# Performance work log

Measured on AMD Instinct MI355X. Metric: run time of the kernel, lower is better.

Reference implementation:

```python
import jax, jax.numpy as jnp
from jax import lax
import numpy as np

NUM_CLASSES = 80
STRIDE = 8
TOPK = 100
SIGAMA = 8.0


def setup_inputs() -> dict:
    key = jax.random.key(0)
    # raw head output: [B, 4+num_classes, H, W]
    x = jax.random.normal(key, (16, 4 + NUM_CLASSES, 160, 160), dtype=jnp.float32)
    return {"input": x}


def _decode(input):
    bs, attrs, H, W = input.shape
    C = attrs - 4
    pred = jnp.transpose(input, (0, 2, 3, 1))  # [B,H,W,4+C]
    x = jax.nn.sigmoid(pred[..., 0])
    y = jax.nn.sigmoid(pred[..., 1])
    w = pred[..., 2]
    h = pred[..., 3]
    pred_cls = jax.nn.sigmoid(pred[..., 4:])  # [B,H,W,C]

    grid_x = jnp.arange(W, dtype=input.dtype)[None, None, :]
    grid_y = jnp.arange(H, dtype=input.dtype)[None, :, None]
    pred_boxes = jnp.stack(
        [x + grid_x, y + grid_y, jnp.exp(w) * SIGAMA, jnp.exp(h) * SIGAMA], axis=-1
    )  # [B,H,W,4]

    # Faithful to F.max_pool2d applied to a [B,H,W,C] tensor: torch pools the
    # LAST TWO dims, i.e. a 5x5 window over (W, C), padding 2, stride 1.
    neg_inf = jnp.array(-jnp.inf, dtype=pred_cls.dtype)
    hmax = lax.reduce_window(
        pred_cls, neg_inf, lax.max,
        window_dimensions=(1, 1, 5, 5),
        window_strides=(1, 1, 1, 1),
        padding=((0, 0), (0, 0), (2, 2), (2, 2)),
    )
    keep = (hmax == pred_cls).astype(pred_cls.dtype)
    pred_cls = pred_cls * keep

    # --- dual top-k (CenterNet-style) ---
    scores = jnp.transpose(pred_cls, (0, 3, 1, 2)).reshape(bs, C, H * W)
    topk_scores, topk_inds = lax.top_k(scores, TOPK)          # [B,C,K] per-class
    topk_score, topk_ind = lax.top_k(topk_scores.reshape(bs, C * TOPK), TOPK)  # [B,K]
    topk_clses = (topk_ind // TOPK).astype(jnp.int32)         # class of each pick
    topk_inds = jnp.take_along_axis(topk_inds.reshape(bs, C * TOPK), topk_ind, axis=1)  # [B,K] spatial idx

    boxes = jnp.take_along_axis(
        pred_boxes.reshape(bs, H * W, 4), topk_inds[:, :, None], axis=1
    )  # [B,K,4]
    cls = jnp.take_along_axis(
        pred_cls.reshape(bs, H * W, C), topk_inds[:, :, None], axis=1
    )  # [B,K,C]
    conf = jnp.ones((bs, TOPK, 1), dtype=input.dtype)
    scale = jnp.array([STRIDE, STRIDE, STRIDE, STRIDE], dtype=input.dtype)
    return jnp.concatenate([boxes * scale, conf, cls], axis=-1)  # [B,K,5+C]


def reference(input):
    return _decode(input)
```

## Files before the change

kernel.cpp:

```cpp
#include <hip/hip_runtime.h>
#include <hip/hip_bf16.h>
#include <cstdint>

#define BATCH 16
#define ATTRS 84
#define NC    80
#define HH    160
#define WW    160
#define HWSZ  (HH * WW)
#define KTOP  100
#define CAP   8192
#define XGATE 2.9444389791664403f
#define LDW   48
#define LCAP  64
#define CSTR  16

__device__ __forceinline__ float sigf(float x) {
    return 1.0f / (1.0f + __expf(-x));
}

__global__ __launch_bounds__(320, 8) void k_nms(const float* __restrict__ in,
                                                unsigned long long* __restrict__ gather,
                                                unsigned int* __restrict__ counts) {
    const int wg  = blockIdx.x;
    const int b   = wg / (HH * 4);
    const int rem = wg % (HH * 4);
    const int h   = rem >> 2;
    const int q   = rem & 3;
    const int t   = (int)threadIdx.x;

    __shared__ float sg[NC][LDW];
    __shared__ unsigned long long lbuf[LCAP];
    __shared__ unsigned int lcount;
    __shared__ unsigned int gbase;

    if (t == 0) lcount = 0;

    const int w0 = q * 40;
    const float* slab = in + ((size_t)b * ATTRS + 4) * HWSZ + (size_t)h * WW + (w0 - 4);

#pragma unroll
    for (int it = 0; it < 3; ++it) {
        const int f4 = it * 320 + t;
        const int c  = f4 / 12;
        const int j4 = f4 % 12;
        const bool oob = (q == 0 && j4 == 0) || (q == 3 && j4 == 11);
        float4 v;
        if (oob) {
            v.x = -INFINITY; v.y = -INFINITY; v.z = -INFINITY; v.w = -INFINITY;
        } else {
            v = *reinterpret_cast<const float4*>(slab + (size_t)c * HWSZ + j4 * 4);
        }
        *reinterpret_cast<float4*>(&sg[c][j4 * 4]) = v;
    }
    __syncthreads();

    const int c    = t % NC;
    const int wq2  = t / NC;
    const int cj0  = 4 + wq2 * 10;

    float s_[14];
#pragma unroll
    for (int k = 0; k < 7; ++k) {
        const float2 v2 = *reinterpret_cast<const float2*>(&sg[c][cj0 - 2 + 2 * k]);
        s_[2 * k + 0] = v2.x;
        s_[2 * k + 1] = v2.y;
    }

    const int r0 = max(c - 2, 0), r1 = max(c - 1, 0);
    const int r3 = min(c + 1, NC - 1), r4 = min(c + 2, NC - 1);

#pragma unroll
    for (int i = 0; i < 10; ++i) {
        const float x = s_[i + 2];
        if (x >= XGATE) {
            const int j = cj0 + i;
            float vm = -INFINITY;
#pragma unroll
            for (int dj = -2; dj <= 2; ++dj) {
                const int jj = j + dj;
                vm = fmaxf(vm, sg[r0][jj]);
                vm = fmaxf(vm, sg[r1][jj]);
                vm = fmaxf(vm, sg[c ][jj]);
                vm = fmaxf(vm, sg[r3][jj]);
                vm = fmaxf(vm, sg[r4][jj]);
            }
            if (x == vm) {
                const float ssc = sigf(x);
                const int w = w0 + wq2 * 10 + i;
                const unsigned idx = (unsigned)(c * HWSZ + h * WW + w);
                unsigned long long key =
                    ((unsigned long long)__float_as_uint(ssc) << 21) |
                    (unsigned long long)(0x1FFFFFu - idx);
                unsigned p = atomicAdd(&lcount, 1u);
                if (p < LCAP) {
                    lbuf[p] = key;
                } else {
                    unsigned g = atomicAdd(&counts[b * CSTR], 1u);
                    if (g < CAP) gather[(size_t)b * CAP + g] = key;
                }
            }
        }
    }
    __syncthreads();

    const unsigned n = min(lcount, (unsigned)LCAP);
    if (t == 0 && n > 0) gbase = atomicAdd(&counts[b * CSTR], n);
    __syncthreads();
    for (unsigned i = t; i < n; i += 320) {
        unsigned g = gbase + i;
        if (g < CAP) gather[(size_t)b * CAP + g] = lbuf[i];
    }
}

__global__ __launch_bounds__(256) void k_select(const unsigned long long* __restrict__ gather,
                                                const unsigned int* __restrict__ counts,
                                                unsigned int* __restrict__ picks) {
    const int b = blockIdx.x;
    const int t = (int)threadIdx.x;

    __shared__ unsigned int hist[2048];
    __shared__ unsigned int chunksum[256];
    __shared__ unsigned long long compact[512];
    __shared__ unsigned int ncompact;
    __shared__ int b2_sh;

    const int M = min(counts[b * CSTR], (unsigned)CAP);
    const unsigned long long* keys = gather + (size_t)b * CAP;

    for (int i = t; i < 2048; i += 256) hist[i] = 0;
    if (t == 0) ncompact = 0;
    __syncthreads();

    for (int i = t; i < M; i += 256) {
        unsigned sb = (unsigned)(keys[i] >> 21);
        int bk = (int)((sb - 0x3F700000u) >> 9);
        bk = min(max(bk, 0), 2047);
        atomicAdd(&hist[bk], 1u);
    }
    __syncthreads();

    unsigned sum = 0;
#pragma unroll
    for (int j = 0; j < 8; ++j) sum += hist[t * 8 + j];
    chunksum[t] = sum;
    __syncthreads();
    for (int off = 1; off < 256; off <<= 1) {
        unsigned v = (t + off < 256) ? chunksum[t + off] : 0u;
        __syncthreads();
        chunksum[t] += v;
        __syncthreads();
    }

    const int target = (M < KTOP) ? M : KTOP;
    if (target > 0 &&
        (int)chunksum[t] >= target && (t == 255 || (int)chunksum[t + 1] < target)) {
        unsigned cum = (t == 255) ? 0u : chunksum[t + 1];
        int bsel = t * 8;
        for (int j = 7; j >= 0; --j) {
            cum += hist[t * 8 + j];
            if ((int)cum >= target) { bsel = t * 8 + j; break; }
        }
        b2_sh = bsel;
    }
    __syncthreads();
    const int b2 = b2_sh;

    for (int i = t; i < M; i += 256) {
        unsigned long long k = keys[i];
        unsigned sb = (unsigned)(k >> 21);
        int bk = min(max((int)((sb - 0x3F700000u) >> 9), 0), 2047);
        if (bk >= b2) {
            unsigned p = atomicAdd(&ncompact, 1u);
            if (p < 512) compact[p] = k;
        }
    }
    __syncthreads();

    const int N = (int)min(ncompact, 512u);
    for (int i = t; i < N; i += 256) {
        unsigned long long ki = compact[i];
        int rank = 0;
        for (int j = 0; j < N; ++j) rank += (compact[j] > ki) ? 1 : 0;
        if (rank < KTOP) {
            unsigned idx = 0x1FFFFFu - (unsigned)(ki & 0x1FFFFFu);
            picks[b * KTOP + rank] = idx % HWSZ;
        }
    }
}

__global__ __launch_bounds__(128) void k_emit(const float* __restrict__ in,
                                              const unsigned int* __restrict__ picks,
                                              float* __restrict__ out) {
    const int pk = blockIdx.x;
    const int b  = pk / KTOP;
    const int t  = (int)threadIdx.x;
    const unsigned hw = picks[pk];
    const int h = (int)(hw / WW), w = (int)(hw % WW);

    __shared__ float tile[NC][5];

    const float* base = in + (size_t)b * ATTRS * HWSZ;

    if (t < NC) {
        const int c = t;
        int a0 = (max(w - 2, 0)) & ~3;
        a0 = min(a0, WW - 8);
        const float* rp = base + (size_t)(4 + c) * HWSZ + (size_t)h * WW;
        const float4 f0 = *reinterpret_cast<const float4*>(rp + a0);
        const float4 f1 = *reinterpret_cast<const float4*>(rp + a0 + 4);
        float sp[8] = { f0.x, f0.y, f0.z, f0.w, f1.x, f1.y, f1.z, f1.w };
#pragma unroll
        for (int j = 0; j < 5; ++j) {
            const int wc = w + j - 2;
            float vv = -INFINITY;
            if (wc >= 0 && wc < WW) vv = sigf(sp[wc - a0]);
            tile[c][j] = vv;
        }
    }
    __syncthreads();

    float* orow = out + (size_t)pk * (5 + NC);

    if (t < 4) {
        float v = base[(size_t)t * HWSZ + hw];
        float r;
        if (t == 0)      r = (sigf(v) + (float)w) * 8.0f;
        else if (t == 1) r = (sigf(v) + (float)h) * 8.0f;
        else             r = expf(v) * 64.0f;
        orow[t] = r;
    }
    if (t == 4) orow[4] = 1.0f;

    if (t < NC) {
        const int c = t;
        const int cl = max(0, c - 2), ch = min(NC - 1, c + 2);
        float m = -INFINITY;
        for (int cc = cl; cc <= ch; ++cc) {
#pragma unroll
            for (int j = 0; j < 5; ++j) m = fmaxf(m, tile[cc][j]);
        }
        float sc = tile[c][2];
        orow[5 + c] = (sc == m) ? sc : 0.0f;
    }
}

extern "C" void kernel_launch(void* const* d_in, const int* in_sizes, int n_in,
                              void* d_out, int out_size, void* d_ws, size_t ws_size,
                              hipStream_t stream) {
    const float* in = (const float*)d_in[0];
    float* out = (float*)d_out;

    unsigned int* counts = (unsigned int*)d_ws;
    unsigned int* picks  = (unsigned int*)((char*)d_ws + 1024);
    unsigned long long* gather = (unsigned long long*)((char*)d_ws + 8192);

    hipMemsetAsync(d_ws, 0, 1024, stream);

    k_nms<<<BATCH * HH * 4, 320, 0, stream>>>(in, gather, counts);
    k_select<<<BATCH, 256, 0, stream>>>(gather, counts, picks);
    k_emit<<<BATCH * KTOP, 128, 0, stream>>>(in, picks, out);
}
```

Before: 230.5 us.

## Stream class planes with flat float4 reads and check rare candidates from global

Replaces the LDS-staged slab NMS, where each workgroup covered one row quarter across all 80 classes, with a flat streaming pass: each workgroup reads a contiguous 64KB chunk of class scores as coalesced float4 loads. Only values above the sigmoid gate (about 0.15% of elements) trigger a 5x5 window check, which reads neighbours straight from global memory through the caches. This removes the strided per-class slab loads, the shared-memory staging and a barrier, and uses far fewer, larger workgroups. The cost is scattered, divergent global reads for candidates and a larger local key buffer.

```diff
diff --git a/kernel.cpp b/kernel.cpp
--- a/kernel.cpp
+++ b/kernel.cpp
@@ -11,93 +11,69 @@
 #define KTOP  100
 #define CAP   8192
 #define XGATE 2.9444389791664403f
-#define LDW   48
-#define LCAP  64
+#define LCAP  192
 #define CSTR  16
+#define CHUNKS 125
 
 __device__ __forceinline__ float sigf(float x) {
     return 1.0f / (1.0f + __expf(-x));
 }
 
-__global__ __launch_bounds__(320, 8) void k_nms(const float* __restrict__ in,
-                                                unsigned long long* __restrict__ gather,
-                                                unsigned int* __restrict__ counts) {
-    const int wg  = blockIdx.x;
-    const int b   = wg / (HH * 4);
-    const int rem = wg % (HH * 4);
-    const int h   = rem >> 2;
-    const int q   = rem & 3;
-    const int t   = (int)threadIdx.x;
-
-    __shared__ float sg[NC][LDW];
+__global__ __launch_bounds__(256) void k_nms(const float* __restrict__ in,
+                                             unsigned long long* __restrict__ gather,
+                                             unsigned int* __restrict__ counts) {
+    const int wg    = blockIdx.x;
+    const int b     = wg / CHUNKS;
+    const int chunk = wg % CHUNKS;
+    const int t     = (int)threadIdx.x;
+
     __shared__ unsigned long long lbuf[LCAP];
     __shared__ unsigned int lcount;
     __shared__ unsigned int gbase;
 
     if (t == 0) lcount = 0;
-
-    const int w0 = q * 40;
-    const float* slab = in + ((size_t)b * ATTRS + 4) * HWSZ + (size_t)h * WW + (w0 - 4);
-
-#pragma unroll
-    for (int it = 0; it < 3; ++it) {
-        const int f4 = it * 320 + t;
-        const int c  = f4 / 12;
-        const int j4 = f4 % 12;
-        const bool oob = (q == 0 && j4 == 0) || (q == 3 && j4 == 11);
-        float4 v;
-        if (oob) {
-            v.x = -INFINITY; v.y = -INFINITY; v.z = -INFINITY; v.w = -INFINITY;
-        } else {
-            v = *reinterpret_cast<const float4*>(slab + (size_t)c * HWSZ + j4 * 4);
-        }
-        *reinterpret_cast<float4*>(&sg[c][j4 * 4]) = v;
-    }
-    __syncthreads();
-
-    const int c    = t % NC;
-    const int wq2  = t / NC;
-    const int cj0  = 4 + wq2 * 10;
-
-    float s_[14];
-#pragma unroll
-    for (int k = 0; k < 7; ++k) {
-        const float2 v2 = *reinterpret_cast<const float2*>(&sg[c][cj0 - 2 + 2 * k]);
-        s_[2 * k + 0] = v2.x;
-        s_[2 * k + 1] = v2.y;
-    }
-
-    const int r0 = max(c - 2, 0), r1 = max(c - 1, 0);
-    const int r3 = min(c + 1, NC - 1), r4 = min(c + 2, NC - 1);
-
-#pragma unroll
-    for (int i = 0; i < 10; ++i) {
-        const float x = s_[i + 2];
-        if (x >= XGATE) {
-            const int j = cj0 + i;
-            float vm = -INFINITY;
-#pragma unroll
-            for (int dj = -2; dj <= 2; ++dj) {
-                const int jj = j + dj;
-                vm = fmaxf(vm, sg[r0][jj]);
-                vm = fmaxf(vm, sg[r1][jj]);
-                vm = fmaxf(vm, sg[c ][jj]);
-                vm = fmaxf(vm, sg[r3][jj]);
-                vm = fmaxf(vm, sg[r4][jj]);
-            }
-            if (x == vm) {
-                const float ssc = sigf(x);
-                const int w = w0 + wq2 * 10 + i;
-                const unsigned idx = (unsigned)(c * HWSZ + h * WW + w);
-                unsigned long long key =
-                    ((unsigned long long)__float_as_uint(ssc) << 21) |
-                    (unsigned long long)(0x1FFFFFu - idx);
-                unsigned p = atomicAdd(&lcount, 1u);
-                if (p < LCAP) {
-                    lbuf[p] = key;
-                } else {
-                    unsigned g = atomicAdd(&counts[b * CSTR], 1u);
-                    if (g < CAP) gather[(size_t)b * CAP + g] = key;
+    __syncthreads();
+
+    const float* slab = in + ((size_t)b * ATTRS + 4) * HWSZ;
+    const int base_f4 = chunk * 4096;
+
+#pragma unroll
+    for (int it = 0; it < 16; ++it) {
+        const int f4 = base_f4 + it * 256 + t;
+        const float4 v = *reinterpret_cast<const float4*>(slab + (size_t)f4 * 4);
+        const float vmax = fmaxf(fmaxf(v.x, v.y), fmaxf(v.z, v.w));
+        if (vmax >= XGATE) {
+#pragma unroll
+            for (int jj = 0; jj < 4; ++jj) {
+                const float x = (&v.x)[jj];
+                if (x >= XGATE) {
+                    const int f = f4 * 4 + jj;
+                    const int c = f / HWSZ;
+                    const int r = f % HWSZ;
+                    const int h = r / WW;
+                    const int w = r % WW;
+                    const int c0 = max(c - 2, 0), c1 = min(c + 2, NC - 1);
+                    const int wl = max(w - 2, 0), wh = min(w + 2, WW - 1);
+                    float vm = -INFINITY;
+                    for (int cc = c0; cc <= c1; ++cc) {
+                        const float* rowp = slab + (size_t)cc * HWSZ + h * WW;
+                        for (int ww = wl; ww <= wh; ++ww) {
+                            vm = fmaxf(vm, rowp[ww]);
+                        }
+                    }
+                    if (x == vm) {
+                        const float ssc = sigf(x);
+                        unsigned long long key =
+                            ((unsigned long long)__float_as_uint(ssc) << 21) |
+                            (unsigned long long)(0x1FFFFFu - (unsigned)f);
+                        unsigned p = atomicAdd(&lcount, 1u);
+                        if (p < LCAP) {
+                            lbuf[p] = key;
+                        } else {
+                            unsigned g = atomicAdd(&counts[b * CSTR], 1u);
+                            if (g < CAP) gather[(size_t)b * CAP + g] = key;
+                        }
+                    }
                 }
             }
         }
@@ -107,7 +83,7 @@
     const unsigned n = min(lcount, (unsigned)LCAP);
     if (t == 0 && n > 0) gbase = atomicAdd(&counts[b * CSTR], n);
     __syncthreads();
-    for (unsigned i = t; i < n; i += 320) {
+    for (unsigned i = t; i < n; i += 256) {
         unsigned g = gbase + i;
         if (g < CAP) gather[(size_t)b * CAP + g] = lbuf[i];
     }
@@ -257,7 +233,7 @@
 
     hipMemsetAsync(d_ws, 0, 1024, stream);
 
-    k_nms<<<BATCH * HH * 4, 320, 0, stream>>>(in, gather, counts);
+    k_nms<<<BATCH * CHUNKS, 256, 0, stream>>>(in, gather, counts);
     k_select<<<BATCH, 256, 0, stream>>>(gather, counts, picks);
     k_emit<<<BATCH * KTOP, 128, 0, stream>>>(in, picks, out);
 }
```

Measured after the change: 281.2 us. +22.0%, slower.
